# Optimization experiments

Measured on AMD Instinct MI355X. Metric: run time of the kernel, lower is better.

The kernel has to match this reference:

```python
import math
import jax, jax.numpy as jnp
import numpy as np

B, N, HID, NH = 4, 1024, 1024, 16
DH = HID // NH
MLP = int(HID * 4.0)


def _ndense(x, w):
    # NormalizedDense: row-normalize kernel (axis=1 for 2D), alpha=sqrt(w[0].size)=sqrt(out),
    # then divide by sqrt(fan_in).
    norm = jnp.linalg.norm(w, axis=1, keepdims=True)
    alpha = jnp.sqrt(jnp.asarray(w.shape[1], x.dtype))
    wn = w / (norm * alpha + 1e-4)
    wn = wn / jnp.sqrt(jnp.asarray(w.shape[0], x.dtype))
    return x @ wn


def mp_silu(x):
    return jax.nn.silu(x) / 0.596


def pixel_norm(x, eps=1e-4):
    return x * jax.lax.rsqrt(jnp.mean(x * x, axis=-1, keepdims=True) + eps)


def mp_add(a, b, t=0.3):
    return ((1 - t) * a + t * b) / math.sqrt((1 - t) ** 2 + t ** 2)


def setup_inputs() -> dict:
    key = jax.random.key(0)
    ks = jax.random.split(key, 9)
    std = 0.02
    return {
        "x": jax.random.normal(ks[0], (B, N, HID), jnp.float32),
        "c": jax.random.normal(ks[1], (B, HID), jnp.float32),
        "w_cond": std * jax.random.normal(ks[2], (HID, 2 * HID), jnp.float32),
        "w_qkv": std * jax.random.normal(ks[3], (HID, 3 * HID), jnp.float32),
        "w_out": std * jax.random.normal(ks[4], (HID, HID), jnp.float32),
        "w_mlp1": std * jax.random.normal(ks[5], (HID, MLP), jnp.float32),
        "w_mlp2": std * jax.random.normal(ks[6], (MLP, HID), jnp.float32),
        "attn_gain": 0.1 * jax.random.normal(ks[7], (), jnp.float32),
        "mlp_gain": 0.1 * jax.random.normal(ks[8], (), jnp.float32),
    }


def reference(x, c, w_cond, w_qkv, w_out, w_mlp1, w_mlp2, attn_gain, mlp_gain):
    # conditioning -> gain/shift
    cc = mp_silu(c)
    cc = _ndense(cc, w_cond)                       # [B, 2H]
    gain, shift = jnp.split(cc, 2, axis=-1)        # [B, H] each

    # attention branch
    x_cond = pixel_norm(x) * (1 + gain[:, None]) + shift[:, None]
    qkv = _ndense(x_cond, w_qkv)                   # [B, N, 3H]
    q, k, v = jnp.split(qkv, 3, axis=-1)
    q, k, v = pixel_norm(q), pixel_norm(k), pixel_norm(v)

    def split_heads(t):
        return t.reshape(B, N, NH, DH).transpose(0, 2, 1, 3)  # [B, NH, N, DH]

    q, k, v = split_heads(q), split_heads(k), split_heads(v)
    q = q / jnp.sqrt(jnp.sum(q * q, axis=-1, keepdims=True) + 1e-6)
    k = k / jnp.sqrt(jnp.sum(k * k, axis=-1, keepdims=True) + 1e-6)

    attn = jnp.einsum('bhnd,bhmd->bhnm', q, k) / math.sqrt(DH)
    attn = jax.nn.softmax(attn, axis=-1)
    x_attn = jnp.einsum('bhnm,bhmd->bhnd', attn, v)
    x_attn = x_attn.transpose(0, 2, 1, 3).reshape(B, N, HID)
    x_attn = pixel_norm(_ndense(x_attn, w_out)) * jnp.exp(attn_gain)
    x = mp_add(x, x_attn, t=0.3)

    # MLP branch
    x_cond = pixel_norm(x) * (1 + gain[:, None]) + shift[:, None]
    h = mp_silu(pixel_norm(_ndense(x_cond, w_mlp1)))
    x_mlp = pixel_norm(_ndense(h, w_mlp2)) * jnp.exp(mlp_gain)
    x = mp_add(x, x_mlp, t=0.3)
    return x
```

## Files before the change

kernel.cpp:

```cpp
#include <hip/hip_runtime.h>

typedef __bf16 bf16_t;
typedef __attribute__((ext_vector_type(8))) __bf16 bh8;
typedef __attribute__((ext_vector_type(4))) __bf16 bh4;
typedef __attribute__((ext_vector_type(4))) float f32x4;

#define DEV static __device__ __forceinline__

typedef __attribute__((address_space(3))) void lds_void;
typedef const __attribute__((address_space(1))) void glb_void;

DEV void async16(const bf16_t* g, bf16_t* l) {
  __builtin_amdgcn_global_load_lds((glb_void*)g, (lds_void*)l, 16, 0, 0);
}

#define GBAR() asm volatile("s_barrier" ::: "memory")
#define VMW(n) asm volatile("s_waitcnt vmcnt(" #n ")" ::: "memory")

DEV f32x4 mfma16(bh8 a, bh8 b, f32x4 c) {
  return __builtin_amdgcn_mfma_f32_16x16x32_bf16(a, b, c, 0, 0, 0);
}

DEV const bf16_t* lds7(const bf16_t* base, int row, int c) {
  return base + row * 64 + ((c ^ (row & 7)) << 3);
}
DEV bf16_t* ldsP(bf16_t* base, int row, int c) {
  int m = (row & 7) ^ ((row >> 3) & 1);
  return base + row * 64 + ((c ^ m) << 3);
}

DEV float wave_sum(float v) {
#pragma unroll
  for (int m = 32; m > 0; m >>= 1) v += __shfl_xor(v, m, 64);
  return v;
}

DEV float block_sum(float v, float* sbuf) {
  v = wave_sum(v);
  int wid = threadIdx.x >> 6;
  if ((threadIdx.x & 63) == 0) sbuf[wid] = v;
  __syncthreads();
  float r = sbuf[0] + sbuf[1] + sbuf[2] + sbuf[3];
  __syncthreads();
  return r;
}

__global__ void k_wnorm_all(const float* __restrict__ w_cond, const float* __restrict__ w_qkv,
                            const float* __restrict__ w_out, const float* __restrict__ w_mlp1,
                            const float* __restrict__ w_mlp2, float* __restrict__ s) {
  __shared__ float sbuf[4];
  int id = blockIdx.x;
  const float* W; int N, K, row;
  if (id < 1024)      { W = w_cond; N = 2048; K = 1024; row = id; }
  else if (id < 2048) { W = w_qkv;  N = 3072; K = 1024; row = id - 1024; }
  else if (id < 3072) { W = w_out;  N = 1024; K = 1024; row = id - 2048; }
  else if (id < 4096) { W = w_mlp1; N = 4096; K = 1024; row = id - 3072; }
  else                { W = w_mlp2; N = 1024; K = 4096; row = id - 4096; }
  const float4* wr = (const float4*)(W + (size_t)row * N);
  float acc = 0.f;
  for (int i = threadIdx.x; i < (N >> 2); i += 256) {
    float4 w = wr[i];
    acc += w.x*w.x + w.y*w.y + w.z*w.z + w.w*w.w;
  }
  float tot = block_sum(acc, sbuf);
  if (threadIdx.x == 0) {
    float norm = sqrtf(tot);
    s[id] = 1.0f / ((norm * sqrtf((float)N) + 1e-4f) * sqrtf((float)K));
  }
}

__global__ void k_wtrans_all(const float* __restrict__ w_cond, const float* __restrict__ w_qkv,
                             const float* __restrict__ w_out, const float* __restrict__ w_mlp1,
                             const float* __restrict__ w_mlp2, const float* __restrict__ sall,
                             bf16_t* __restrict__ wt_cond, bf16_t* __restrict__ wt_qkv,
                             bf16_t* __restrict__ wt_out, bf16_t* __restrict__ wt_mlp1,
                             bf16_t* __restrict__ wt_mlp2) {
  __shared__ float tile[64][65];
  int id = blockIdx.x;
  const float* W; const float* s; bf16_t* Wt; int K, N, n0, k0;
  if (id < 512)       { W=w_cond; s=sall;      Wt=wt_cond; K=1024; N=2048; int l=id;      n0=(l&31)*64; k0=(l>>5)*64; }
  else if (id < 1280) { W=w_qkv;  s=sall+1024; Wt=wt_qkv;  K=1024; N=3072; int l=id-512;  n0=(l%48)*64; k0=(l/48)*64; }
  else if (id < 1536) { W=w_out;  s=sall+2048; Wt=wt_out;  K=1024; N=1024; int l=id-1280; n0=(l&15)*64; k0=(l>>4)*64; }
  else if (id < 2560) { W=w_mlp1; s=sall+3072; Wt=wt_mlp1; K=1024; N=4096; int l=id-1536; n0=(l&63)*64; k0=(l>>6)*64; }
  else                { W=w_mlp2; s=sall+4096; Wt=wt_mlp2; K=4096; N=1024; int l=id-2560; n0=(l&15)*64; k0=(l>>4)*64; }
  int t = threadIdx.x;
#pragma unroll
  for (int i = t; i < 1024; i += 256) {
    int r = i >> 4, c4 = (i & 15) << 2;
    float sc = s[k0 + r];
    float4 w = *(const float4*)(W + (size_t)(k0 + r) * N + n0 + c4);
    tile[r][c4 + 0] = w.x * sc;
    tile[r][c4 + 1] = w.y * sc;
    tile[r][c4 + 2] = w.z * sc;
    tile[r][c4 + 3] = w.w * sc;
  }
  __syncthreads();
#pragma unroll
  for (int i = t; i < 1024; i += 256) {
    int rr = i >> 4, cc = (i & 15) << 2;
    bh4 o;
    o[0] = (bf16_t)tile[cc + 0][rr];
    o[1] = (bf16_t)tile[cc + 1][rr];
    o[2] = (bf16_t)tile[cc + 2][rr];
    o[3] = (bf16_t)tile[cc + 3][rr];
    *(bh4*)(Wt + (size_t)(n0 + rr) * K + k0 + cc) = o;
  }
}

__global__ void k_cond(const float* __restrict__ c, const bf16_t* __restrict__ wt,
                       float* __restrict__ gs) {
  __shared__ float cc[4][1024];
  int t = threadIdx.x;
  for (int i = t; i < 4096; i += 256) {
    int b = i >> 10, col = i & 1023;
    float x = c[b * 1024 + col];
    float sig = 1.f / (1.f + __expf(-x));
    cc[b][col] = x * sig * (1.f / 0.596f);
  }
  __syncthreads();
  int wid = t >> 6, lane = t & 63;
  int j = blockIdx.x * 4 + wid;
  const bf16_t* wr = wt + (size_t)j * 1024;
  float acc0 = 0, acc1 = 0, acc2 = 0, acc3 = 0;
  for (int i = lane; i < 1024; i += 64) {
    float w = (float)wr[i];
    acc0 += cc[0][i] * w; acc1 += cc[1][i] * w;
    acc2 += cc[2][i] * w; acc3 += cc[3][i] * w;
  }
  float v0 = wave_sum(acc0), v1 = wave_sum(acc1), v2 = wave_sum(acc2), v3 = wave_sum(acc3);
  if (lane == 0) {
    gs[0 * 2048 + j] = v0; gs[1 * 2048 + j] = v1;
    gs[2 * 2048 + j] = v2; gs[3 * 2048 + j] = v3;
  }
}

__global__ void k_xcond(const float* __restrict__ x, const float* __restrict__ gs,
                        bf16_t* __restrict__ xc) {
  __shared__ float sbuf[4];
  int row = blockIdx.x, b = row >> 10, t = threadIdx.x;
  float4 v = ((const float4*)(x + (size_t)row * 1024))[t];
  float ss = v.x*v.x + v.y*v.y + v.z*v.z + v.w*v.w;
  float tot = block_sum(ss, sbuf);
  float r = rsqrtf(tot * (1.f/1024.f) + 1e-4f);
  float4 g  = ((const float4*)(gs + b * 2048))[t];
  float4 sh = ((const float4*)(gs + b * 2048 + 1024))[t];
  bh4 o;
  o[0] = (bf16_t)(v.x * r * (1.f + g.x) + sh.x);
  o[1] = (bf16_t)(v.y * r * (1.f + g.y) + sh.y);
  o[2] = (bf16_t)(v.z * r * (1.f + g.z) + sh.z);
  o[3] = (bf16_t)(v.w * r * (1.f + g.w) + sh.w);
  *(bh4*)(xc + (size_t)row * 1024 + t * 4) = o;
}

__global__ __launch_bounds__(512, 2) void k_gemm8(const bf16_t* __restrict__ A,
                                                  const bf16_t* __restrict__ Bt,
                                                  bf16_t* __restrict__ C,
                                                  int M, int N, int K, int klen) {
  __shared__ __attribute__((aligned(16))) bf16_t As[2][2][256][32];
  __shared__ __attribute__((aligned(16))) bf16_t Bs[2][2][256][32];
  const int ntn = gridDim.x;
  const unsigned flat = blockIdx.x + ntn * blockIdx.y;
  const unsigned q = (ntn * gridDim.y) >> 3;
  const unsigned wg = (flat & 7) * q + (flat >> 3);
  const int m0 = (int)(wg / (unsigned)ntn) * 256;
  const int n0 = (int)(wg % (unsigned)ntn) * 256;
  const size_t kbeg = (size_t)blockIdx.z * klen;
  C += (size_t)blockIdx.z * M * N;
  const int t = threadIdx.x, lane = t & 63;
  const int wm = (t >> 6) >> 2, wn = (t >> 6) & 3;
  const int l15 = lane & 15, quad = lane >> 4;
  const int q8 = (quad ^ ((l15 >> 2) & 2)) * 8;
  const int rA = wm * 128 + l15;
  const int rB = wn * 64 + l15;
  const int sr = t >> 2;
  const int sc = ((t & 3) << 3) ^ ((t & 32) >> 1);
  const int swv = (t >> 6) * 512;
  const bf16_t* AgS = A + (size_t)(m0 + sr) * K + kbeg + sc;
  const bf16_t* BgS = Bt + (size_t)(n0 + sr) * K + kbeg + sc;
  const size_t rstep = (size_t)128 * K;
  const int NT = klen >> 6;
  f32x4 acc[8][4] = {};

#define STG_A(kt_, h_, bb_) { const bf16_t* g = AgS + (kt_) * 64 + (h_) * 32; \
    bf16_t* l = &As[bb_][h_][0][0] + swv; async16(g, l); async16(g + rstep, l + 4096); }
#define STG_B(kt_, h_, bb_) { const bf16_t* g = BgS + (kt_) * 64 + (h_) * 32; \
    bf16_t* l = &Bs[bb_][h_][0][0] + swv; async16(g, l); async16(g + rstep, l + 4096); }

  STG_B(0, 0, 0); STG_B(0, 1, 0);
  STG_A(0, 0, 0); STG_A(0, 1, 0);
  if (NT > 1) { STG_B(1, 0, 1); STG_B(1, 1, 1); VMW(4); } else { VMW(0); }
  GBAR();

  for (int kt = 0; kt < NT; ++kt) {
    const int bb = kt & 1;
    bh8 a[4][2], b[4][2];
#pragma unroll
    for (int m = 0; m < 4; ++m)
#pragma unroll
      for (int kc = 0; kc < 2; ++kc)
        a[m][kc] = *(const bh8*)&As[bb][kc][rA + m * 16][q8];
#pragma unroll
    for (int n = 0; n < 2; ++n)
#pragma unroll
      for (int kc = 0; kc < 2; ++kc)
        b[n][kc] = *(const bh8*)&Bs[bb][kc][rB + n * 16][q8];
    if (kt + 1 < NT) STG_A(kt + 1, 0, bb ^ 1);
    GBAR();
    __builtin_amdgcn_s_setprio(1);
#pragma unroll
    for (int m = 0; m < 4; ++m)
#pragma unroll
      for (int n = 0; n < 2; ++n)
#pragma unroll
        for (int kc = 0; kc < 2; ++kc)
          acc[m][n] = mfma16(a[m][kc], b[n][kc], acc[m][n]);
    __builtin_amdgcn_s_setprio(0);
    GBAR();
#pragma unroll
    for (int n = 0; n < 2; ++n)
#pragma unroll
      for (int kc = 0; kc < 2; ++kc)
        b[2 + n][kc] = *(const bh8*)&Bs[bb][kc][rB + (2 + n) * 16][q8];
    if (kt + 1 < NT) STG_A(kt + 1, 1, bb ^ 1);
    GBAR();
    __builtin_amdgcn_s_setprio(1);
#pragma unroll
    for (int m = 0; m < 4; ++m)
#pragma unroll
      for (int n = 0; n < 2; ++n)
#pragma unroll
        for (int kc = 0; kc < 2; ++kc)
          acc[m][2 + n] = mfma16(a[m][kc], b[2 + n][kc], acc[m][2 + n]);
    __builtin_amdgcn_s_setprio(0);
    GBAR();
#pragma unroll
    for (int m = 0; m < 4; ++m)
#pragma unroll
      for (int kc = 0; kc < 2; ++kc)
        a[m][kc] = *(const bh8*)&As[bb][kc][rA + 64 + m * 16][q8];
    if (kt + 2 < NT) STG_B(kt + 2, 0, bb);
    GBAR();
    __builtin_amdgcn_s_setprio(1);
#pragma unroll
    for (int m = 0; m < 4; ++m)
#pragma unroll
      for (int n = 0; n < 2; ++n)
#pragma unroll
        for (int kc = 0; kc < 2; ++kc)
          acc[4 + m][n] = mfma16(a[m][kc], b[n][kc], acc[4 + m][n]);
    __builtin_amdgcn_s_setprio(0);
    GBAR();
    if (kt + 2 < NT) STG_B(kt + 2, 1, bb);
    __builtin_amdgcn_s_setprio(1);
#pragma unroll
    for (int m = 0; m < 4; ++m)
#pragma unroll
      for (int n = 0; n < 2; ++n)
#pragma unroll
        for (int kc = 0; kc < 2; ++kc)
          acc[4 + m][2 + n] = mfma16(a[m][kc], b[2 + n][kc], acc[4 + m][2 + n]);
    __builtin_amdgcn_s_setprio(0);
    if (kt + 2 < NT) { VMW(4); } else { VMW(0); }
    GBAR();
  }
#undef STG_A
#undef STG_B

  const int cm = m0 + wm * 128 + quad * 4;
  const int cn = n0 + wn * 64 + l15;
#pragma unroll
  for (int m = 0; m < 8; ++m)
#pragma unroll
    for (int n = 0; n < 4; ++n)
#pragma unroll
      for (int r2 = 0; r2 < 4; ++r2)
        C[(size_t)(cm + m * 16 + r2) * N + cn + n * 16] = (bf16_t)acc[m][n][r2];
}

__global__ void k_qkvnorm(const bf16_t* __restrict__ qkv, bf16_t* __restrict__ qo,
                          bf16_t* __restrict__ ko, float* __restrict__ rsv) {
  __shared__ float sbuf[4];
  const int row = blockIdx.x, b = row >> 10, n = row & 1023, t = threadIdx.x;
  const bf16_t* rp = qkv + (size_t)row * 3072;
  bh4 q4 = *(const bh4*)(rp + t * 4);
  bh4 k4 = *(const bh4*)(rp + 1024 + t * 4);
  bh4 v4 = *(const bh4*)(rp + 2048 + t * 4);
  float4 q = {(float)q4[0], (float)q4[1], (float)q4[2], (float)q4[3]};
  float4 k = {(float)k4[0], (float)k4[1], (float)k4[2], (float)k4[3]};
  float4 v = {(float)v4[0], (float)v4[1], (float)v4[2], (float)v4[3]};
  float sq = q.x*q.x + q.y*q.y + q.z*q.z + q.w*q.w;
  float sk = k.x*k.x + k.y*k.y + k.z*k.z + k.w*k.w;
  float sv = v.x*v.x + v.y*v.y + v.z*v.z + v.w*v.w;
  float tq = block_sum(sq, sbuf);
  float tk = block_sum(sk, sbuf);
  float tv = block_sum(sv, sbuf);
  float rq = rsqrtf(tq * (1.f/1024.f) + 1e-4f);
  float rk = rsqrtf(tk * (1.f/1024.f) + 1e-4f);
  float rv = rsqrtf(tv * (1.f/1024.f) + 1e-4f);
  float hq = sq, hk = sk;
#pragma unroll
  for (int m = 1; m < 16; m <<= 1) { hq += __shfl_xor(hq, m, 64); hk += __shfl_xor(hk, m, 64); }
  float qs = rq * rsqrtf(rq*rq*hq + 1e-6f);
  float ks = rk * rsqrtf(rk*rk*hk + 1e-6f);
  int h = t >> 4, d = (t & 15) * 4;
  size_t base = ((size_t)(b * 16 + h) * 1024 + n) * 64 + d;
  bh4 oq, okk;
  oq[0]=(bf16_t)(q.x*qs); oq[1]=(bf16_t)(q.y*qs); oq[2]=(bf16_t)(q.z*qs); oq[3]=(bf16_t)(q.w*qs);
  okk[0]=(bf16_t)(k.x*ks); okk[1]=(bf16_t)(k.y*ks); okk[2]=(bf16_t)(k.z*ks); okk[3]=(bf16_t)(k.w*ks);
  *(bh4*)(qo + base) = oq;
  *(bh4*)(ko + base) = okk;
  if (t == 0) rsv[row] = rv;
}

__global__ void k_vtrans(const bf16_t* __restrict__ qkv, const float* __restrict__ rsv,
                         bf16_t* __restrict__ vt) {
  __shared__ bf16_t tile[64][72];
  const int n0 = blockIdx.x * 64, bh = blockIdx.y;
  const int b = bh >> 4, h = bh & 15;
  const int t = threadIdx.x;
  const bf16_t* src = qkv + ((size_t)(b * 1024 + n0)) * 3072 + 2048 + h * 64;
#pragma unroll
  for (int i = t; i < 512; i += 256) {
    int r = i >> 3, p = (i & 7) * 8;
    float sc = rsv[b * 1024 + n0 + r];
    bh8 vv = *(const bh8*)(src + (size_t)r * 3072 + p);
    bh8 o8;
#pragma unroll
    for (int j = 0; j < 8; j++) o8[j] = (bf16_t)((float)vv[j] * sc);
    *(bh8*)&tile[r][p] = o8;
  }
  __syncthreads();
  bf16_t* dst = vt + (size_t)bh * 64 * 1024 + n0;
#pragma unroll
  for (int i = t; i < 512; i += 256) {
    int d = i & 63, nch = (i >> 6) * 8;
    bh8 o;
#pragma unroll
    for (int j = 0; j < 8; j++) o[j] = tile[nch + j][d];
    *(bh8*)(dst + (size_t)d * 1024 + nch) = o;
  }
}

__global__ __launch_bounds__(256, 2) void k_attn(const bf16_t* __restrict__ Q,
                                                 const bf16_t* __restrict__ K,
                                                 const bf16_t* __restrict__ Vt_g,
                                                 bf16_t* __restrict__ O) {
  __shared__ __attribute__((aligned(16))) bf16_t Qs[128][64];
  __shared__ __attribute__((aligned(16))) bf16_t Ks[2][64][64];
  __shared__ __attribute__((aligned(16))) bf16_t Vt[2][64][64];
  __shared__ __attribute__((aligned(16))) bf16_t Ps[128][64];
  const unsigned flat = blockIdx.x + 8u * blockIdx.y;
  const int qt = (int)((flat >> 3) & 7);
  const int bh = (int)((flat & 7) * 8 + (flat >> 6));
  const int b = bh >> 4, h = bh & 15;
  const int t = threadIdx.x, lane = t & 63, wid = t >> 6;
  const int l15 = lane & 15, quad = lane >> 4;
  const int strip = wid * 32;
  const int srow = t >> 3;
  const int scol = ((t & 7) ^ (srow & 7)) << 3;
  const int swv = wid * 512;
  const bf16_t* Qg = Q + ((size_t)bh * 1024 + qt * 128) * 64;
  const bf16_t* Kg = K + (size_t)bh * 1024 * 64;
  const bf16_t* Vg = Vt_g + (size_t)bh * 64 * 1024;

#pragma unroll
  for (int c2 = 0; c2 < 4; ++c2)
    async16(Qg + (size_t)(c2 * 32 + srow) * 64 + scol, &Qs[0][0] + c2 * 2048 + swv);
#pragma unroll
  for (int r0 = 0; r0 < 64; r0 += 32) {
    async16(Kg + (size_t)(r0 + srow) * 64 + scol, &Ks[0][0][0] + r0 * 64 + swv);
    async16(Vg + (size_t)(r0 + srow) * 1024 + scol, &Vt[0][0][0] + r0 * 64 + swv);
  }
  VMW(0);
  GBAR();

  f32x4 o[2][4] = {};
  float rs[2][4] = {{}, {}};
  for (int kt = 0; kt < 16; ++kt) {
    const int bb = kt & 1;
    const int kv0 = kt * 64;
    if (kt < 15) {
#pragma unroll
      for (int r0 = 0; r0 < 64; r0 += 32) {
        async16(Kg + (size_t)(kv0 + 64 + r0 + srow) * 64 + scol,
                &Ks[bb ^ 1][0][0] + r0 * 64 + swv);
        async16(Vg + (size_t)(r0 + srow) * 1024 + kv0 + 64 + scol,
                &Vt[bb ^ 1][0][0] + r0 * 64 + swv);
      }
    }
    f32x4 s[2][4] = {};
    bh8 aq[2][2], bk[4][2];
#pragma unroll
    for (int rf = 0; rf < 2; ++rf)
#pragma unroll
      for (int kc = 0; kc < 2; ++kc)
        aq[rf][kc] = *(const bh8*)lds7(&Qs[0][0], strip + rf * 16 + l15, kc * 4 + quad);
#pragma unroll
    for (int j = 0; j < 4; ++j)
#pragma unroll
      for (int kc = 0; kc < 2; ++kc)
        bk[j][kc] = *(const bh8*)lds7(&Ks[bb][0][0], j * 16 + l15, kc * 4 + quad);
    __builtin_amdgcn_s_setprio(1);
#pragma unroll
    for (int rf = 0; rf < 2; ++rf)
#pragma unroll
      for (int j = 0; j < 4; ++j)
#pragma unroll
        for (int kc = 0; kc < 2; ++kc)
          s[rf][j] = mfma16(aq[rf][kc], bk[j][kc], s[rf][j]);
    __builtin_amdgcn_s_setprio(0);
#pragma unroll
    for (int rf = 0; rf < 2; ++rf)
#pragma unroll
      for (int j = 0; j < 4; ++j)
#pragma unroll
        for (int r = 0; r < 4; ++r) {
          float p = __expf(s[rf][j][r] * 0.125f);
          bf16_t pb = (bf16_t)p;
          rs[rf][r] += (float)pb;
          int prow = strip + rf * 16 + quad * 4 + r;
          ldsP(&Ps[0][0], prow, j * 2 + (l15 >> 3))[l15 & 7] = pb;
        }
    bh8 ap[2][2], bv[4][2];
#pragma unroll
    for (int rf = 0; rf < 2; ++rf)
#pragma unroll
      for (int kc = 0; kc < 2; ++kc)
        ap[rf][kc] = *(const bh8*)ldsP(&Ps[0][0], strip + rf * 16 + l15, kc * 4 + quad);
#pragma unroll
    for (int j = 0; j < 4; ++j)
#pragma unroll
      for (int kc = 0; kc < 2; ++kc)
        bv[j][kc] = *(const bh8*)lds7(&Vt[bb][0][0], j * 16 + l15, kc * 4 + quad);
    __builtin_amdgcn_s_setprio(1);
#pragma unroll
    for (int rf = 0; rf < 2; ++rf)
#pragma unroll
      for (int j = 0; j < 4; ++j)
#pragma unroll
        for (int kc = 0; kc < 2; ++kc)
          o[rf][j] = mfma16(ap[rf][kc], bv[j][kc], o[rf][j]);
    __builtin_amdgcn_s_setprio(0);
    if (kt < 15) { VMW(0); GBAR(); }
  }
#pragma unroll
  for (int rf = 0; rf < 2; ++rf)
#pragma unroll
    for (int r = 0; r < 4; ++r) {
      float v = rs[rf][r];
      v += __shfl_xor(v, 1, 64); v += __shfl_xor(v, 2, 64);
      v += __shfl_xor(v, 4, 64); v += __shfl_xor(v, 8, 64);
      float inv = 1.f / v;
      int n = qt * 128 + strip + rf * 16 + quad * 4 + r;
#pragma unroll
      for (int j = 0; j < 4; ++j)
        O[((size_t)b * 1024 + n) * 1024 + h * 64 + j * 16 + l15] = (bf16_t)(o[rf][j][r] * inv);
    }
}

__global__ void k_amerge(const bf16_t* __restrict__ y, const float* __restrict__ x,
                         const float* __restrict__ gs, const float* __restrict__ again,
                         bf16_t* __restrict__ x1, bf16_t* __restrict__ xc2) {
  __shared__ float sbuf[4];
  int row = blockIdx.x, b = row >> 10, t = threadIdx.x;
  const size_t PS = (size_t)4096 * 1024;
  float4 yv = {0.f, 0.f, 0.f, 0.f};
#pragma unroll
  for (int p = 0; p < 4; p++) {
    bh4 a = *(const bh4*)(y + p * PS + (size_t)row * 1024 + t * 4);
    yv.x += (float)a[0]; yv.y += (float)a[1]; yv.z += (float)a[2]; yv.w += (float)a[3];
  }
  float4 xv = ((const float4*)(x + (size_t)row * 1024))[t];
  float ss = yv.x*yv.x + yv.y*yv.y + yv.z*yv.z + yv.w*yv.w;
  float tot = block_sum(ss, sbuf);
  float r = rsqrtf(tot * (1.f/1024.f) + 1e-4f);
  float ag = __expf(again[0]);
  const float C1 = 0.7f / 0.76157731059f, C2 = 0.3f / 0.76157731059f;
  float4 xo;
  xo.x = C1 * xv.x + C2 * (yv.x * r * ag);
  xo.y = C1 * xv.y + C2 * (yv.y * r * ag);
  xo.z = C1 * xv.z + C2 * (yv.z * r * ag);
  xo.w = C1 * xv.w + C2 * (yv.w * r * ag);
  bh4 x1o;
  x1o[0] = (bf16_t)xo.x; x1o[1] = (bf16_t)xo.y; x1o[2] = (bf16_t)xo.z; x1o[3] = (bf16_t)xo.w;
  *(bh4*)(x1 + (size_t)row * 1024 + t * 4) = x1o;
  float ss1 = xo.x*xo.x + xo.y*xo.y + xo.z*xo.z + xo.w*xo.w;
  float tot1 = block_sum(ss1, sbuf);
  float r1 = rsqrtf(tot1 * (1.f/1024.f) + 1e-4f);
  float4 g  = ((const float4*)(gs + b * 2048))[t];
  float4 sh = ((const float4*)(gs + b * 2048 + 1024))[t];
  bh4 o;
  o[0] = (bf16_t)(xo.x * r1 * (1.f + g.x) + sh.x);
  o[1] = (bf16_t)(xo.y * r1 * (1.f + g.y) + sh.y);
  o[2] = (bf16_t)(xo.z * r1 * (1.f + g.z) + sh.z);
  o[3] = (bf16_t)(xo.w * r1 * (1.f + g.w) + sh.w);
  *(bh4*)(xc2 + (size_t)row * 1024 + t * 4) = o;
}

__global__ void k_mlpnorm(const bf16_t* __restrict__ hf, bf16_t* __restrict__ hb) {
  __shared__ float sbuf[4];
  int row = blockIdx.x, t = threadIdx.x;
  const bf16_t* rp = hf + (size_t)row * 4096;
  float4 v[4]; float ss = 0.f;
#pragma unroll
  for (int i = 0; i < 4; i++) {
    bh4 bv = *(const bh4*)(rp + (t + 256 * i) * 4);
    v[i].x = (float)bv[0]; v[i].y = (float)bv[1]; v[i].z = (float)bv[2]; v[i].w = (float)bv[3];
    ss += v[i].x*v[i].x + v[i].y*v[i].y + v[i].z*v[i].z + v[i].w*v[i].w;
  }
  float tot = block_sum(ss, sbuf);
  float r = rsqrtf(tot * (1.f/4096.f) + 1e-4f);
#pragma unroll
  for (int i = 0; i < 4; i++) {
    float a[4] = {v[i].x, v[i].y, v[i].z, v[i].w};
    bh4 o;
#pragma unroll
    for (int j = 0; j < 4; j++) {
      float u = a[j] * r;
      float sig = 1.f / (1.f + __expf(-u));
      o[j] = (bf16_t)(u * sig * (1.f / 0.596f));
    }
    *(bh4*)(hb + (size_t)row * 4096 + (t + 256 * i) * 4) = o;
  }
}

__global__ void k_fmerge(const bf16_t* __restrict__ y, const bf16_t* __restrict__ x1,
                         const float* __restrict__ mgain, float* __restrict__ out) {
  __shared__ float sbuf[4];
  int row = blockIdx.x, t = threadIdx.x;
  const size_t PS = (size_t)4096 * 1024;
  float4 yv = {0.f, 0.f, 0.f, 0.f};
#pragma unroll
  for (int p = 0; p < 4; p++) {
    bh4 yp = *(const bh4*)(y + p * PS + (size_t)row * 1024 + t * 4);
    yv.x += (float)yp[0]; yv.y += (float)yp[1]; yv.z += (float)yp[2]; yv.w += (float)yp[3];
  }
  bh4 xb = *(const bh4*)(x1 + (size_t)row * 1024 + t * 4);
  float4 xv = {(float)xb[0], (float)xb[1], (float)xb[2], (float)xb[3]};
  float ss = yv.x*yv.x + yv.y*yv.y + yv.z*yv.z + yv.w*yv.w;
  float tot = block_sum(ss, sbuf);
  float r = rsqrtf(tot * (1.f/1024.f) + 1e-4f);
  float mg = __expf(mgain[0]);
  const float C1 = 0.7f / 0.76157731059f, C2 = 0.3f / 0.76157731059f;
  float4 o;
  o.x = C1 * xv.x + C2 * (yv.x * r * mg);
  o.y = C1 * xv.y + C2 * (yv.y * r * mg);
  o.z = C1 * xv.z + C2 * (yv.z * r * mg);
  o.w = C1 * xv.w + C2 * (yv.w * r * mg);
  ((float4*)(out + (size_t)row * 1024))[t] = o;
}

extern "C" void kernel_launch(void* const* d_in, const int* in_sizes, int n_in,
                              void* d_out, int out_size, void* d_ws, size_t ws_size,
                              hipStream_t stream) {
  const float* x      = (const float*)d_in[0];
  const float* c      = (const float*)d_in[1];
  const float* w_cond = (const float*)d_in[2];
  const float* w_qkv  = (const float*)d_in[3];
  const float* w_out  = (const float*)d_in[4];
  const float* w_mlp1 = (const float*)d_in[5];
  const float* w_mlp2 = (const float*)d_in[6];
  const float* again  = (const float*)d_in[7];
  const float* mgain  = (const float*)d_in[8];
  float* out = (float*)d_out;
  char* ws = (char*)d_ws;

  bf16_t* wt_cond = (bf16_t*)(ws + 0);
  bf16_t* wt_qkv  = (bf16_t*)(ws + 4194304);
  bf16_t* wt_out  = (bf16_t*)(ws + 10485760);
  bf16_t* wt_mlp1 = (bf16_t*)(ws + 12582912);
  bf16_t* wt_mlp2 = (bf16_t*)(ws + 20971520);
  float*  sn      = (float*)(ws + 29360128);
  float*  gs      = (float*)(ws + 29392896);
  bf16_t* xc      = (bf16_t*)(ws + 29425664);
  bf16_t* qh      = (bf16_t*)(ws + 37814272);
  bf16_t* kh      = (bf16_t*)(ws + 46202880);
  float*  rsv     = (float*)(ws + 54591488);
  bf16_t* xattn   = (bf16_t*)(ws + 62980096);
  bf16_t* hb      = (bf16_t*)(ws + 37814272);
  bf16_t* x1      = (bf16_t*)(ws + 71368704);
  bf16_t* vt      = (bf16_t*)(ws + 79757312);
  bf16_t* buf_b   = (bf16_t*)(ws + 88145920);

  k_wnorm_all<<<8192, 256, 0, stream>>>(w_cond, w_qkv, w_out, w_mlp1, w_mlp2, sn);
  k_wtrans_all<<<3584, 256, 0, stream>>>(w_cond, w_qkv, w_out, w_mlp1, w_mlp2, sn,
                                         wt_cond, wt_qkv, wt_out, wt_mlp1, wt_mlp2);

  k_cond<<<512, 256, 0, stream>>>(c, wt_cond, gs);
  k_xcond<<<4096, 256, 0, stream>>>(x, gs, xc);
  k_gemm8<<<dim3(12, 16, 1), 512, 0, stream>>>(xc, wt_qkv, buf_b, 4096, 3072, 1024, 1024);
  k_qkvnorm<<<4096, 256, 0, stream>>>(buf_b, qh, kh, rsv);
  k_vtrans<<<dim3(16, 64), 256, 0, stream>>>(buf_b, rsv, vt);
  k_attn<<<dim3(8, 64), 256, 0, stream>>>(qh, kh, vt, xattn);
  k_gemm8<<<dim3(4, 16, 4), 512, 0, stream>>>(xattn, wt_out, buf_b, 4096, 1024, 1024, 256);
  k_amerge<<<4096, 256, 0, stream>>>(buf_b, x, gs, again, x1, xc);
  k_gemm8<<<dim3(16, 16, 1), 512, 0, stream>>>(xc, wt_mlp1, buf_b, 4096, 4096, 1024, 1024);
  k_mlpnorm<<<4096, 256, 0, stream>>>(buf_b, hb);
  k_gemm8<<<dim3(4, 16, 4), 512, 0, stream>>>(hb, wt_mlp2, buf_b, 4096, 1024, 4096, 1024);
  k_fmerge<<<4096, 256, 0, stream>>>(buf_b, x1, mgain, out);
  (void)in_sizes; (void)n_in; (void)out_size; (void)ws_size;
}
```

Measured before the change: 362.0 us.

## Replace split-K out-projection GEMM with 128x128-tile kernel, drop partial-sum merge

Adds a new 256-thread GEMM kernel with 128x128 tiles, double-buffered async LDS staging and a two-phase MFMA schedule. It computes the attention output projection in one pass over K instead of four split-K partial slices. The merge kernel now reads a single result row instead of summing four bf16 partials, which cuts the partial-sum traffic. The trade-off is less K-parallelism per tile, in exchange for 256 blocks with two per CU.

```diff
diff --git a/kernel.cpp b/kernel.cpp
--- a/kernel.cpp
+++ b/kernel.cpp
@@ -277,6 +277,95 @@
         C[(size_t)(cm + m * 16 + r2) * N + cn + n * 16] = (bf16_t)acc[m][n][r2];
 }
 
+__global__ __launch_bounds__(256, 2) void k_gemm2ph(const bf16_t* __restrict__ A,
+                                                    const bf16_t* __restrict__ Bt,
+                                                    bf16_t* __restrict__ C,
+                                                    int M, int N, int K) {
+  __shared__ __attribute__((aligned(16))) bf16_t As[2][2][128][32];
+  __shared__ __attribute__((aligned(16))) bf16_t Bs[2][2][128][32];
+  const int ntn = gridDim.x;
+  const unsigned flat = blockIdx.x + ntn * blockIdx.y;
+  const unsigned q = (ntn * gridDim.y) >> 3;
+  const unsigned wg = (flat & 7) * q + (flat >> 3);
+  const int m0 = (int)(wg / (unsigned)ntn) * 128;
+  const int n0 = (int)(wg % (unsigned)ntn) * 128;
+  const int t = threadIdx.x, lane = t & 63;
+  const int wm = (t >> 6) >> 1, wn = (t >> 6) & 1;
+  const int l15 = lane & 15, quad = lane >> 4;
+  const int q8 = (quad ^ ((l15 >> 2) & 2)) * 8;
+  const int rA = wm * 64 + l15;
+  const int rB = wn * 64 + l15;
+  const int sr = t >> 2;
+  const int sc = ((t & 3) << 3) ^ ((t & 32) >> 1);
+  const int swv = (t >> 6) * 512;
+  const bf16_t* AgS = A + (size_t)(m0 + sr) * K + sc;
+  const bf16_t* BgS = Bt + (size_t)(n0 + sr) * K + sc;
+  const size_t rstep = (size_t)64 * K;
+  const int NT = K >> 6;
+  f32x4 acc[4][4] = {};
+
+#define STG_A(kt_, h_, bb_) { const bf16_t* g = AgS + (kt_) * 64 + (h_) * 32; \
+    bf16_t* l = &As[bb_][h_][0][0] + swv; async16(g, l); async16(g + rstep, l + 2048); }
+#define STG_B(kt_, h_, bb_) { const bf16_t* g = BgS + (kt_) * 64 + (h_) * 32; \
+    bf16_t* l = &Bs[bb_][h_][0][0] + swv; async16(g, l); async16(g + rstep, l + 2048); }
+
+  STG_B(0, 0, 0); STG_B(0, 1, 0);
+  STG_A(0, 0, 0); STG_A(0, 1, 0);
+  if (NT > 1) { STG_B(1, 0, 1); STG_B(1, 1, 1); VMW(4); } else { VMW(0); }
+  GBAR();
+
+  for (int kt = 0; kt < NT; ++kt) {
+    const int bb = kt & 1;
+    bh8 a[4][2], b[4][2];
+#pragma unroll
+    for (int m = 0; m < 4; ++m)
+#pragma unroll
+      for (int kc = 0; kc < 2; ++kc)
+        a[m][kc] = *(const bh8*)&As[bb][kc][rA + m * 16][q8];
+#pragma unroll
+    for (int n = 0; n < 4; ++n)
+#pragma unroll
+      for (int kc = 0; kc < 2; ++kc)
+        b[n][kc] = *(const bh8*)&Bs[bb][kc][rB + n * 16][q8];
+    if (kt + 1 < NT) { STG_A(kt + 1, 0, bb ^ 1); STG_A(kt + 1, 1, bb ^ 1); }
+    GBAR();
+    __builtin_amdgcn_s_setprio(1);
+#pragma unroll
+    for (int m = 0; m < 4; ++m)
+#pragma unroll
+      for (int n = 0; n < 2; ++n)
+#pragma unroll
+        for (int kc = 0; kc < 2; ++kc)
+          acc[m][n] = mfma16(a[m][kc], b[n][kc], acc[m][n]);
+    __builtin_amdgcn_s_setprio(0);
+    GBAR();
+    if (kt + 2 < NT) { STG_B(kt + 2, 0, bb); STG_B(kt + 2, 1, bb); }
+    __builtin_amdgcn_s_setprio(1);
+#pragma unroll
+    for (int m = 0; m < 4; ++m)
+#pragma unroll
+      for (int n = 0; n < 2; ++n)
+#pragma unroll
+        for (int kc = 0; kc < 2; ++kc)
+          acc[m][2 + n] = mfma16(a[m][kc], b[2 + n][kc], acc[m][2 + n]);
+    __builtin_amdgcn_s_setprio(0);
+    if (kt + 2 < NT) { VMW(4); } else { VMW(0); }
+    GBAR();
+  }
+#undef STG_A
+#undef STG_B
+
+  const int cm = m0 + wm * 64 + quad * 4;
+  const int cn = n0 + wn * 64 + l15;
+#pragma unroll
+  for (int m = 0; m < 4; ++m)
+#pragma unroll
+    for (int n = 0; n < 4; ++n)
+#pragma unroll
+      for (int r2 = 0; r2 < 4; ++r2)
+        C[(size_t)(cm + m * 16 + r2) * N + cn + n * 16] = (bf16_t)acc[m][n][r2];
+}
+
 __global__ void k_qkvnorm(const bf16_t* __restrict__ qkv, bf16_t* __restrict__ qo,
                           bf16_t* __restrict__ ko, float* __restrict__ rsv) {
   __shared__ float sbuf[4];
@@ -463,13 +552,8 @@
                          bf16_t* __restrict__ x1, bf16_t* __restrict__ xc2) {
   __shared__ float sbuf[4];
   int row = blockIdx.x, b = row >> 10, t = threadIdx.x;
-  const size_t PS = (size_t)4096 * 1024;
-  float4 yv = {0.f, 0.f, 0.f, 0.f};
-#pragma unroll
-  for (int p = 0; p < 4; p++) {
-    bh4 a = *(const bh4*)(y + p * PS + (size_t)row * 1024 + t * 4);
-    yv.x += (float)a[0]; yv.y += (float)a[1]; yv.z += (float)a[2]; yv.w += (float)a[3];
-  }
+  bh4 a = *(const bh4*)(y + (size_t)row * 1024 + t * 4);
+  float4 yv = {(float)a[0], (float)a[1], (float)a[2], (float)a[3]};
   float4 xv = ((const float4*)(x + (size_t)row * 1024))[t];
   float ss = yv.x*yv.x + yv.y*yv.y + yv.z*yv.z + yv.w*yv.w;
   float tot = block_sum(ss, sbuf);
@@ -592,7 +676,7 @@
   k_qkvnorm<<<4096, 256, 0, stream>>>(buf_b, qh, kh, rsv);
   k_vtrans<<<dim3(16, 64), 256, 0, stream>>>(buf_b, rsv, vt);
   k_attn<<<dim3(8, 64), 256, 0, stream>>>(qh, kh, vt, xattn);
-  k_gemm8<<<dim3(4, 16, 4), 512, 0, stream>>>(xattn, wt_out, buf_b, 4096, 1024, 1024, 256);
+  k_gemm2ph<<<dim3(8, 32), 256, 0, stream>>>(xattn, wt_out, buf_b, 4096, 1024, 1024);
   k_amerge<<<4096, 256, 0, stream>>>(buf_b, x, gs, again, x1, xc);
   k_gemm8<<<dim3(16, 16, 1), 512, 0, stream>>>(xc, wt_mlp1, buf_b, 4096, 4096, 1024, 1024);
   k_mlpnorm<<<4096, 256, 0, stream>>>(buf_b, hb);
```

After: 352.9 us. 1.03x faster.
